# Kernel tuning notes

Measured on AMD Instinct MI355X. Metric: run time of the kernel, lower is better.

## Reference

```python
import jax, jax.numpy as jnp
import numpy as np


def _sage(x_src, x_dst, si, di, wl, b, wr):
    # out = x_dst @ wl^T + b  (self projection)
    out = x_dst @ wl.T + b
    n_dst = x_dst.shape[0]
    # mean aggregation of gathered source features over destination nodes
    agg = jax.ops.segment_sum(x_src[si], di, num_segments=n_dst)  # [N_dst, D]
    cnt = jax.ops.segment_sum(jnp.ones(si.shape, x_src.dtype), di, num_segments=n_dst)
    agg = agg / jnp.maximum(cnt, 1.0)[:, None]
    out = out + agg @ wr.T
    # F.normalize(p=2, dim=-1) with eps=1e-12
    norm = jnp.linalg.norm(out, axis=-1, keepdims=True)
    return out / jnp.maximum(norm, 1e-12)


def setup_inputs() -> dict:
    key = jax.random.key(0)
    ks = jax.random.split(key, 32)
    NA, NE, NF, D, E = 100000, 200000, 100000, 128, 400000
    inp = {
        'x_article': jax.random.normal(ks[0], (NA, D), jnp.float32),
        'x_entity': jax.random.normal(ks[1], (NE, D), jnp.float32),
        'x_fact': jax.random.normal(ks[2], (NF, D), jnp.float32),
    }
    # edge indices per EDGE_TYPES order
    srcs = [NA, NA, NE, NE, NF]
    dsts = [NE, NF, NA, NF, NE]
    for i in range(5):
        inp[f'si{i}'] = jax.random.randint(ks[3 + 2 * i], (E,), 0, srcs[i], jnp.int32)
        inp[f'di{i}'] = jax.random.randint(ks[4 + 2 * i], (E,), 0, dsts[i], jnp.int32)
    # per-edge-type params: W_l [out,in], b [out], W_r [out,in]
    scale = 1.0 / np.sqrt(D)
    for i in range(5):
        inp[f'wl{i}'] = jax.random.normal(ks[13 + 3 * i], (D, D), jnp.float32) * scale
        inp[f'b{i}'] = jnp.zeros((D,), jnp.float32)
        inp[f'wr{i}'] = jax.random.normal(ks[14 + 3 * i], (D, D), jnp.float32) * scale
    return inp


def reference(x_article, x_entity, x_fact,
              si0, di0, si1, di1, si2, di2, si3, di3, si4, di4,
              wl0, b0, wr0, wl1, b1, wr1, wl2, b2, wr2,
              wl3, b3, wr3, wl4, b4, wr4):
    # EDGE_TYPES: (article->entity), (article->fact), (entity->article),
    #             (entity->fact), (fact->entity); contributions to same dst are summed
    out_entity = _sage(x_article, x_entity, si0, di0, wl0, b0, wr0)
    out_fact = _sage(x_article, x_fact, si1, di1, wl1, b1, wr1)
    out_article = _sage(x_entity, x_article, si2, di2, wl2, b2, wr2)
    out_fact = out_fact + _sage(x_entity, x_fact, si3, di3, wl3, b3, wr3)
    out_entity = out_entity + _sage(x_fact, x_entity, si4, di4, wl4, b4, wr4)
    return out_article, out_entity, out_fact
```

## Files before the change

### kernel.cpp

```cpp
#include <hip/hip_runtime.h>
#include <hip/hip_bf16.h>

typedef __bf16 bf16;
typedef __attribute__((ext_vector_type(8))) __bf16 bf16x8;
typedef __attribute__((ext_vector_type(4))) float f32x4;

static __device__ inline bf16x8 pack_bf16x8(f32x4 lo, f32x4 hi) {
    bf16x8 t;
#pragma unroll
    for (int j = 0; j < 4; ++j) {
        t[j]     = (__bf16)lo[j];
        t[4 + j] = (__bf16)hi[j];
    }
    return t;
}

struct WConvArgs { const float* w[10]; bf16* dst; };

__global__ __launch_bounds__(256)
void convert_w(WConvArgs A) {
    int mat = blockIdx.y;
    int tid = blockIdx.x * 256 + threadIdx.x;
    if (tid >= 2048) return;
    int m  = tid & 15;
    int q  = (tid >> 4) & 3;
    int kc = (tid >> 6) & 3;
    int ct = tid >> 8;
    const float* src = A.w[mat] + (size_t)(ct * 16 + m) * 128 + kc * 32 + q * 8;
    bf16x8 t;
#pragma unroll
    for (int j = 0; j < 8; ++j) t[j] = (__bf16)src[j];
    bf16* dst = A.dst + (size_t)mat * 16384 + ((ct * 4 + kc) * 4 + q) * 128 + m * 8;
    *(bf16x8*)dst = t;
}

struct XConvArgs { const float* src[3]; bf16* dst[3]; long long n8[3]; };

__global__ __launch_bounds__(256)
void convert_x(XConvArgs A) {
    int a = blockIdx.y;
    const float* s = A.src[a];
    bf16* d = A.dst[a];
    long long n8 = A.n8[a];
    for (long long i = blockIdx.x * 256LL + threadIdx.x; i < n8;
         i += (long long)gridDim.x * 256) {
        const f32x4* p = (const f32x4*)(s + i * 8);
        ((bf16x8*)d)[i] = pack_bf16x8(p[0], p[1]);
    }
}

struct CsrArgs {
    const int* si[5];
    const int* di[5];
    int* ofs[5];
    int* tick[5];
    int* esrc[5];
    int* bsum[5];
    int E[5];
    int n1[5];
};

__global__ __launch_bounds__(256)
void csr_zero(CsrArgs A) {
    int t = blockIdx.y;
    int i = blockIdx.x * 256 + threadIdx.x;
    if (i < A.n1[t]) A.ofs[t][i] = 0;
}

__global__ __launch_bounds__(256)
void csr_hist(CsrArgs A) {
    int t = blockIdx.y;
    int E = A.E[t];
    const int* di = A.di[t];
    int* ofs = A.ofs[t];
    for (int i = blockIdx.x * 256 + threadIdx.x; i < E; i += gridDim.x * 256)
        atomicAdd(&ofs[di[i] + 1], 1);
}

__global__ __launch_bounds__(256)
void csr_scan_blocks(CsrArgs A) {
    __shared__ int lds[256];
    int ty = blockIdx.y;
    int n = A.n1[ty];
    int* a = A.ofs[ty];
    int* bsum = A.bsum[ty];
    int t = threadIdx.x;
    int base = blockIdx.x * 2048 + t * 8;
    int v[8];
    int run = 0;
#pragma unroll
    for (int j = 0; j < 8; ++j) {
        int idx = base + j;
        int x = (idx < n) ? a[idx] : 0;
        run += x;
        v[j] = run;
    }
    lds[t] = run;
    __syncthreads();
#pragma unroll
    for (int off = 1; off < 256; off <<= 1) {
        int x = (t >= off) ? lds[t - off] : 0;
        __syncthreads();
        lds[t] += x;
        __syncthreads();
    }
    int excl = t ? lds[t - 1] : 0;
#pragma unroll
    for (int j = 0; j < 8; ++j) {
        int idx = base + j;
        if (idx < n) a[idx] = v[j] + excl;
    }
    if (t == 255) bsum[blockIdx.x] = lds[255];
}

__global__ __launch_bounds__(256)
void csr_scan_bsums(CsrArgs A, int nb) {
    __shared__ int lds[256];
    int ty = blockIdx.x;
    int* bsum = A.bsum[ty];
    int t = threadIdx.x;
    int carry = 0;
    for (int base = 0; base < nb; base += 256) {
        int i = base + t;
        int v = (i < nb) ? bsum[i] : 0;
        lds[t] = v;
        __syncthreads();
#pragma unroll
        for (int off = 1; off < 256; off <<= 1) {
            int x = (t >= off) ? lds[t - off] : 0;
            __syncthreads();
            lds[t] += x;
            __syncthreads();
        }
        int excl = t ? lds[t - 1] : 0;
        if (i < nb) bsum[i] = excl + carry;
        carry += lds[255];
        __syncthreads();
    }
}

__global__ __launch_bounds__(256)
void csr_scan_add(CsrArgs A) {
    int ty = blockIdx.y;
    int n = A.n1[ty];
    int* a = A.ofs[ty];
    const int* bsum = A.bsum[ty];
    int* tick = A.tick[ty];
    int i = blockIdx.x * 256 + threadIdx.x;
    if (i < n) {
        int v = a[i] + bsum[i >> 11];
        a[i] = v;
        if (i < n - 1) tick[i] = v;
    }
}

__global__ __launch_bounds__(256)
void csr_fill(CsrArgs A) {
    int ty = blockIdx.y;
    int E = A.E[ty];
    const int* si = A.si[ty];
    const int* di = A.di[ty];
    int* tick = A.tick[ty];
    int* esrc = A.esrc[ty];
    for (int i = blockIdx.x * 256 + threadIdx.x; i < E; i += gridDim.x * 256) {
        int pos = atomicAdd(&tick[di[i]], 1);
        pos = pos < 0 ? 0 : (pos >= E ? E - 1 : pos);
        esrc[pos] = si[i];
    }
}

struct SageAll {
    int bend[3];
    int nd[3];
    int nc[3];
    const float* xdst_f[3];
    const bf16*  xdst_b[3];
    float* out[3];
    const float* xsrc_f[3][2];
    const bf16*  xsrc_b[3][2];
    const int* ofs[3][2];
    const int* esrc[3][2];
    const bf16* wf[3][2];
    const float* bias[3][2];
    int nsrc[3][2];
    int E[3][2];
};

template<int BF16S>
__global__ __launch_bounds__(256)
void sage_all(SageAll A) {
    int bid = blockIdx.x;
    int g = (bid >= A.bend[0]) + (bid >= A.bend[1]);
    int bloc = bid - (g ? A.bend[g - 1] : 0);
    int lane = threadIdx.x & 63;
    int wave = threadIdx.x >> 6;
    int m = lane & 15;
    int q = lane >> 4;
    int nd = A.nd[g];
    int r0 = bloc * 64 + wave * 16;
    int rl = min(r0 + m, nd - 1);

    bf16x8 a1[4];
    if constexpr (BF16S) {
        const bf16x8* xr = (const bf16x8*)(A.xdst_b[g] + (size_t)rl * 128);
#pragma unroll
        for (int kc = 0; kc < 4; ++kc) a1[kc] = xr[kc * 4 + q];
    } else {
        const f32x4* xrow = (const f32x4*)(A.xdst_f[g] + (size_t)rl * 128);
#pragma unroll
        for (int kc = 0; kc < 4; ++kc)
            a1[kc] = pack_bf16x8(xrow[kc * 8 + q * 2], xrow[kc * 8 + q * 2 + 1]);
    }

    float ysum[8][4];
#pragma unroll
    for (int ct = 0; ct < 8; ++ct)
#pragma unroll
        for (int r = 0; r < 4; ++r) ysum[ct][r] = 0.f;

    int nc = A.nc[g];
    for (int c = 0; c < nc; ++c) {
        const int* ofs  = A.ofs[g][c];
        const int* esrc = A.esrc[g][c];
        int nsrc = A.nsrc[g][c];
        int Et   = A.E[g][c];

        int start = ofs[rl];
        int end   = ofs[rl + 1];
        start = start < 0 ? 0 : (start > Et ? Et : start);
        end   = end < start ? start : (end > Et ? Et : end);

        f32x4 aglo[4], aghi[4];
#pragma unroll
        for (int kc = 0; kc < 4; ++kc) {
            aglo[kc] = (f32x4){0.f, 0.f, 0.f, 0.f};
            aghi[kc] = (f32x4){0.f, 0.f, 0.f, 0.f};
        }

        int e = start;
        if constexpr (BF16S) {
            const bf16* xs = A.xsrc_b[g][c];
            for (; e + 2 <= end; e += 2) {
                int s0 = esrc[e], s1 = esrc[e + 1];
                s0 = s0 < 0 ? 0 : (s0 >= nsrc ? nsrc - 1 : s0);
                s1 = s1 < 0 ? 0 : (s1 >= nsrc ? nsrc - 1 : s1);
                const bf16x8* p0 = (const bf16x8*)(xs + (size_t)s0 * 128);
                const bf16x8* p1 = (const bf16x8*)(xs + (size_t)s1 * 128);
#pragma unroll
                for (int kc = 0; kc < 4; ++kc) {
                    bf16x8 v0 = p0[kc * 4 + q];
                    bf16x8 v1 = p1[kc * 4 + q];
#pragma unroll
                    for (int j = 0; j < 4; ++j) {
                        aglo[kc][j] += (float)v0[j] + (float)v1[j];
                        aghi[kc][j] += (float)v0[4 + j] + (float)v1[4 + j];
                    }
                }
            }
            if (e < end) {
                int s0 = esrc[e];
                s0 = s0 < 0 ? 0 : (s0 >= nsrc ? nsrc - 1 : s0);
                const bf16x8* p0 = (const bf16x8*)(xs + (size_t)s0 * 128);
#pragma unroll
                for (int kc = 0; kc < 4; ++kc) {
                    bf16x8 v0 = p0[kc * 4 + q];
#pragma unroll
                    for (int j = 0; j < 4; ++j) {
                        aglo[kc][j] += (float)v0[j];
                        aghi[kc][j] += (float)v0[4 + j];
                    }
                }
            }
        } else {
            const float* xs = A.xsrc_f[g][c];
            for (; e + 2 <= end; e += 2) {
                int s0 = esrc[e], s1 = esrc[e + 1];
                s0 = s0 < 0 ? 0 : (s0 >= nsrc ? nsrc - 1 : s0);
                s1 = s1 < 0 ? 0 : (s1 >= nsrc ? nsrc - 1 : s1);
                const f32x4* p0 = (const f32x4*)(xs + (size_t)s0 * 128 + q * 8);
                const f32x4* p1 = (const f32x4*)(xs + (size_t)s1 * 128 + q * 8);
#pragma unroll
                for (int kc = 0; kc < 4; ++kc) {
                    aglo[kc] += p0[kc * 8] + p1[kc * 8];
                    aghi[kc] += p0[kc * 8 + 1] + p1[kc * 8 + 1];
                }
            }
            if (e < end) {
                int s0 = esrc[e];
                s0 = s0 < 0 ? 0 : (s0 >= nsrc ? nsrc - 1 : s0);
                const f32x4* p0 = (const f32x4*)(xs + (size_t)s0 * 128 + q * 8);
#pragma unroll
                for (int kc = 0; kc < 4; ++kc) {
                    aglo[kc] += p0[kc * 8];
                    aghi[kc] += p0[kc * 8 + 1];
                }
            }
        }

        float invc = 1.0f / (float)max(end - start, 1);
        bf16x8 a2[4];
#pragma unroll
        for (int kc = 0; kc < 4; ++kc) {
            bf16x8 t;
#pragma unroll
            for (int j = 0; j < 4; ++j) {
                t[j]     = (__bf16)(aglo[kc][j] * invc);
                t[4 + j] = (__bf16)(aghi[kc][j] * invc);
            }
            a2[kc] = t;
        }

        const bf16x8* wf = (const bf16x8*)A.wf[g][c];
        int fb = q * 16 + m;
        f32x4 acc[8];
#pragma unroll
        for (int ct = 0; ct < 8; ++ct) {
            f32x4 cc = {0.f, 0.f, 0.f, 0.f};
#pragma unroll
            for (int kc = 0; kc < 4; ++kc) {
                bf16x8 bl = wf[(ct * 4 + kc) * 64 + fb];
                bf16x8 br = wf[2048 + (ct * 4 + kc) * 64 + fb];
                cc = __builtin_amdgcn_mfma_f32_16x16x32_bf16(a1[kc], bl, cc, 0, 0, 0);
                cc = __builtin_amdgcn_mfma_f32_16x16x32_bf16(a2[kc], br, cc, 0, 0, 0);
            }
            acc[ct] = cc;
        }

        const float* bias = A.bias[g][c];
        float ss[4] = {0.f, 0.f, 0.f, 0.f};
#pragma unroll
        for (int ct = 0; ct < 8; ++ct) {
            float bb = bias[ct * 16 + m];
#pragma unroll
            for (int r = 0; r < 4; ++r) {
                float v = acc[ct][r] + bb;
                acc[ct][r] = v;
                ss[r] += v * v;
            }
        }
#pragma unroll
        for (int off = 1; off < 16; off <<= 1) {
#pragma unroll
            for (int r = 0; r < 4; ++r) ss[r] += __shfl_xor(ss[r], off);
        }
        float sc[4];
#pragma unroll
        for (int r = 0; r < 4; ++r) sc[r] = 1.0f / fmaxf(sqrtf(ss[r]), 1e-12f);
#pragma unroll
        for (int ct = 0; ct < 8; ++ct)
#pragma unroll
            for (int r = 0; r < 4; ++r) ysum[ct][r] += acc[ct][r] * sc[r];
    }

#pragma unroll
    for (int r = 0; r < 4; ++r) {
        int orow = r0 + q * 4 + r;
        if (orow < nd) {
            float* op = A.out[g] + (size_t)orow * 128 + m;
#pragma unroll
            for (int ct = 0; ct < 8; ++ct) op[ct * 16] = ysum[ct][r];
        }
    }
}

extern "C" void kernel_launch(void* const* d_in, const int* in_sizes, int n_in,
                              void* d_out, int out_size, void* d_ws, size_t ws_size,
                              hipStream_t stream) {
    const int D = 128;
    const float* xarr[3] = {(const float*)d_in[0], (const float*)d_in[1],
                            (const float*)d_in[2]};
    int NA = in_sizes[0] / D;
    int NE = in_sizes[1] / D;
    int NF = in_sizes[2] / D;
    int nrow[3] = {NA, NE, NF};

    const int* si[5];
    const int* di[5];
    int Et[5];
    for (int i = 0; i < 5; ++i) {
        si[i] = (const int*)d_in[3 + 2 * i];
        di[i] = (const int*)d_in[4 + 2 * i];
        Et[i] = in_sizes[3 + 2 * i];
    }
    const float *wl[5], *bia[5], *wr[5];
    for (int i = 0; i < 5; ++i) {
        wl[i]  = (const float*)d_in[13 + 3 * i];
        bia[i] = (const float*)d_in[14 + 3 * i];
        wr[i]  = (const float*)d_in[15 + 3 * i];
    }

    float* outp = (float*)d_out;
    float* grp_out[3] = {outp, outp + (size_t)NA * D, outp + (size_t)(NA + NE) * D};

    int xsrc_idx[5] = {0, 0, 1, 1, 2};
    int ndst[5]     = {NE, NF, NA, NF, NE};
    int grp_types[3][2] = {{2, -1}, {0, 4}, {1, 3}};
    int grp_nt[3]  = {1, 2, 2};
    int grp_nd[3]  = {NA, NE, NF};
    int grp_dst[3] = {0, 1, 2};

    size_t wf_bytes = (size_t)5 * 32768 * sizeof(bf16);
    size_t csr_all_ints = 0;
    for (int t = 0; t < 5; ++t)
        csr_all_ints += (size_t)(ndst[t] + 1) + ndst[t] + Et[t] + 128;
    size_t xb_elems = ((size_t)NA + NE + NF) * D;

    size_t off_csr = (wf_bytes + 15) & ~(size_t)15;
    size_t off_xb  = (off_csr + csr_all_ints * 4 + 15) & ~(size_t)15;
    int mode_full = (off_xb + xb_elems * sizeof(bf16)) <= ws_size;
    int mode_lean = (off_csr + csr_all_ints * 4) <= ws_size;

    bf16* wfrag = (bf16*)d_ws;
    WConvArgs wa;
    for (int t = 0; t < 5; ++t) {
        wa.w[t * 2]     = wl[t];
        wa.w[t * 2 + 1] = wr[t];
    }
    wa.dst = wfrag;
    convert_w<<<dim3(8, 10), 256, 0, stream>>>(wa);

    bf16* xb = (bf16*)((char*)d_ws + off_xb);
    bf16* xb_arr[3] = {xb, xb + (size_t)NA * D, xb + ((size_t)NA + NE) * D};
    if (mode_full) {
        XConvArgs xa;
        for (int a = 0; a < 3; ++a) {
            xa.src[a] = xarr[a];
            xa.dst[a] = xb_arr[a];
            xa.n8[a]  = (long long)nrow[a] * 16;
        }
        convert_x<<<dim3(2048, 3), 256, 0, stream>>>(xa);
    }

    int* type_ofs[5];
    int* type_esrc[5];
    auto run_csr = [&](const int* types, int nt, int* base) {
        CsrArgs ca = {};
        int* p = base;
        int max_n1 = 0;
        for (int k = 0; k < nt; ++k) {
            int t = types[k];
            int nd = ndst[t], n1 = nd + 1, E = Et[t];
            ca.si[k] = si[t];
            ca.di[k] = di[t];
            ca.ofs[k]  = p; p += n1;
            ca.tick[k] = p; p += nd;
            ca.esrc[k] = p; p += E;
            ca.bsum[k] = p; p += 128;
            ca.E[k] = E;
            ca.n1[k] = n1;
            if (n1 > max_n1) max_n1 = n1;
            type_ofs[t]  = ca.ofs[k];
            type_esrc[t] = ca.esrc[k];
        }
        int blk = (max_n1 + 255) / 256;
        int nb  = (max_n1 + 2047) / 2048;
        csr_zero<<<dim3(blk, nt), 256, 0, stream>>>(ca);
        csr_hist<<<dim3(1024, nt), 256, 0, stream>>>(ca);
        csr_scan_blocks<<<dim3(nb, nt), 256, 0, stream>>>(ca);
        csr_scan_bsums<<<dim3(nt), 256, 0, stream>>>(ca, nb);
        csr_scan_add<<<dim3(blk, nt), 256, 0, stream>>>(ca);
        csr_fill<<<dim3(1024, nt), 256, 0, stream>>>(ca);
    };

    auto fill_group = [&](SageAll& sa, int slot, int g) {
        sa.nd[slot] = grp_nd[g];
        sa.nc[slot] = grp_nt[g];
        sa.xdst_f[slot] = xarr[grp_dst[g]];
        sa.xdst_b[slot] = xb_arr[grp_dst[g]];
        sa.out[slot] = grp_out[g];
        for (int c = 0; c < grp_nt[g]; ++c) {
            int t = grp_types[g][c];
            sa.xsrc_f[slot][c] = xarr[xsrc_idx[t]];
            sa.xsrc_b[slot][c] = xb_arr[xsrc_idx[t]];
            sa.ofs[slot][c]  = type_ofs[t];
            sa.esrc[slot][c] = type_esrc[t];
            sa.wf[slot][c]   = wfrag + (size_t)t * 32768;
            sa.bias[slot][c] = bia[t];
            sa.nsrc[slot][c] = nrow[xsrc_idx[t]];
            sa.E[slot][c]    = Et[t];
        }
    };

    int* csr_base = (int*)((char*)d_ws + off_csr);

    if (mode_lean) {
        int all_types[5] = {0, 1, 2, 3, 4};
        run_csr(all_types, 5, csr_base);

        SageAll sa = {};
        int cum = 0;
        for (int g = 0; g < 3; ++g) {
            fill_group(sa, g, g);
            cum += (grp_nd[g] + 63) / 64;
            sa.bend[g] = cum;
        }
        if (mode_full)
            sage_all<1><<<cum, 256, 0, stream>>>(sa);
        else
            sage_all<0><<<cum, 256, 0, stream>>>(sa);
    } else {
        for (int g = 0; g < 3; ++g) {
            run_csr(grp_types[g], grp_nt[g], csr_base);
            SageAll sa = {};
            fill_group(sa, 0, g);
            int nb = (grp_nd[g] + 63) / 64;
            sa.bend[0] = nb; sa.bend[1] = nb; sa.bend[2] = nb;
            sage_all<0><<<nb, 256, 0, stream>>>(sa);
        }
    }
}
```

Before: 982.1 us.

## Replace CSR build with fixed-capacity per-destination buckets plus overflow list

```diff
diff --git a/kernel.cpp b/kernel.cpp
--- a/kernel.cpp
+++ b/kernel.cpp
@@ -46,6 +46,243 @@
          i += (long long)gridDim.x * 256) {
         const f32x4* p = (const f32x4*)(s + i * 8);
         ((bf16x8*)d)[i] = pack_bf16x8(p[0], p[1]);
+    }
+}
+
+struct FillArgs {
+    const int* si[5];
+    const int* di[5];
+    int* tick[5];
+    int* bucket[5];
+    int2* ovf[5];
+    int* ovfn[5];
+    int E[5];
+    int nd[5];
+    int C;
+};
+
+__global__ __launch_bounds__(256)
+void bkt_zero(FillArgs A) {
+    int t = blockIdx.y;
+    int nd = A.nd[t];
+    int* tick = A.tick[t];
+    for (int i = blockIdx.x * 256 + threadIdx.x; i < nd; i += gridDim.x * 256)
+        tick[i] = 0;
+    if (blockIdx.x == 0 && threadIdx.x == 0) *A.ovfn[t] = 0;
+}
+
+__global__ __launch_bounds__(256)
+void bkt_fill(FillArgs A) {
+    int t = blockIdx.y;
+    int E = A.E[t];
+    int nd = A.nd[t];
+    int C = A.C;
+    const int* si = A.si[t];
+    const int* di = A.di[t];
+    int* tick = A.tick[t];
+    int* bucket = A.bucket[t];
+    int2* ovf = A.ovf[t];
+    int* ovfn = A.ovfn[t];
+    for (int i = blockIdx.x * 256 + threadIdx.x; i < E; i += gridDim.x * 256) {
+        int d = di[i];
+        int s = si[i];
+        d = d < 0 ? 0 : (d >= nd ? nd - 1 : d);
+        int pos = atomicAdd(&tick[d], 1);
+        if (pos >= 0 && pos < C) {
+            bucket[(size_t)d * C + pos] = s;
+        } else {
+            int o = atomicAdd(ovfn, 1);
+            if (o >= 0 && o < E) ovf[o] = make_int2(d, s);
+        }
+    }
+}
+
+template<int BF16S>
+static __device__ inline void accum_src(const float* xf, const bf16* xb,
+                                        int s, int q, f32x4* aglo, f32x4* aghi) {
+    if constexpr (BF16S) {
+        const bf16x8* p = (const bf16x8*)(xb + (size_t)s * 128);
+#pragma unroll
+        for (int kc = 0; kc < 4; ++kc) {
+            bf16x8 v = p[kc * 4 + q];
+#pragma unroll
+            for (int j = 0; j < 4; ++j) {
+                aglo[kc][j] += (float)v[j];
+                aghi[kc][j] += (float)v[4 + j];
+            }
+        }
+    } else {
+        const f32x4* p = (const f32x4*)(xf + (size_t)s * 128 + q * 8);
+#pragma unroll
+        for (int kc = 0; kc < 4; ++kc) {
+            aglo[kc] += p[kc * 8];
+            aghi[kc] += p[kc * 8 + 1];
+        }
+    }
+}
+
+struct SageB {
+    int bend[3];
+    int nd[3];
+    int nc[3];
+    const float* xdst_f[3];
+    const bf16*  xdst_b[3];
+    float* out[3];
+    const float* xsrc_f[3][2];
+    const bf16*  xsrc_b[3][2];
+    const int* tick[3][2];
+    const int* bucket[3][2];
+    const int2* ovf[3][2];
+    const int* ovfn[3][2];
+    const bf16* wf[3][2];
+    const float* bias[3][2];
+    int nsrc[3][2];
+    int ovfcap[3][2];
+};
+
+template<int C, int BF16S>
+__global__ __launch_bounds__(256)
+void sage_bkt(SageB A) {
+    int bid = blockIdx.x;
+    int g = (bid >= A.bend[0]) + (bid >= A.bend[1]);
+    int bloc = bid - (g ? A.bend[g - 1] : 0);
+    int lane = threadIdx.x & 63;
+    int wave = threadIdx.x >> 6;
+    int m = lane & 15;
+    int q = lane >> 4;
+    int nd = A.nd[g];
+    int r0 = bloc * 64 + wave * 16;
+    int rl = min(r0 + m, nd - 1);
+
+    bf16x8 a1[4];
+    if constexpr (BF16S) {
+        const bf16x8* xr = (const bf16x8*)(A.xdst_b[g] + (size_t)rl * 128);
+#pragma unroll
+        for (int kc = 0; kc < 4; ++kc) a1[kc] = xr[kc * 4 + q];
+    } else {
+        const f32x4* xrow = (const f32x4*)(A.xdst_f[g] + (size_t)rl * 128);
+#pragma unroll
+        for (int kc = 0; kc < 4; ++kc)
+            a1[kc] = pack_bf16x8(xrow[kc * 8 + q * 2], xrow[kc * 8 + q * 2 + 1]);
+    }
+
+    float ysum[8][4];
+#pragma unroll
+    for (int ct = 0; ct < 8; ++ct)
+#pragma unroll
+        for (int r = 0; r < 4; ++r) ysum[ct][r] = 0.f;
+
+    int nc = A.nc[g];
+    for (int c = 0; c < nc; ++c) {
+        const float* xf = A.xsrc_f[g][c];
+        const bf16*  xb = A.xsrc_b[g][c];
+        int nsrc = A.nsrc[g][c];
+
+        int deg = A.tick[g][c][rl];
+        deg = deg < 0 ? 0 : deg;
+        int dc = deg < C ? deg : C;
+        const int* brow = A.bucket[g][c] + (size_t)rl * C;
+
+        f32x4 aglo[4], aghi[4];
+#pragma unroll
+        for (int kc = 0; kc < 4; ++kc) {
+            aglo[kc] = (f32x4){0.f, 0.f, 0.f, 0.f};
+            aghi[kc] = (f32x4){0.f, 0.f, 0.f, 0.f};
+        }
+
+#pragma unroll
+        for (int t0 = 0; t0 < C; t0 += 4) {
+            if (t0 < dc) {
+                int4 s4 = *(const int4*)(brow + t0);
+                int ss[4] = {s4.x, s4.y, s4.z, s4.w};
+#pragma unroll
+                for (int u = 0; u < 4; ++u) {
+                    if (t0 + u < dc) {
+                        int s = ss[u];
+                        s = s < 0 ? 0 : (s >= nsrc ? nsrc - 1 : s);
+                        accum_src<BF16S>(xf, xb, s, q, aglo, aghi);
+                    }
+                }
+            }
+        }
+        if (deg > C) {
+            int on = *A.ovfn[g][c];
+            int cap = A.ovfcap[g][c];
+            on = on < 0 ? 0 : (on > cap ? cap : on);
+            const int2* ov = A.ovf[g][c];
+            for (int i = 0; i < on; ++i) {
+                int2 ds = ov[i];
+                if (ds.x == rl) {
+                    int s = ds.y;
+                    s = s < 0 ? 0 : (s >= nsrc ? nsrc - 1 : s);
+                    accum_src<BF16S>(xf, xb, s, q, aglo, aghi);
+                }
+            }
+        }
+
+        float invc = 1.0f / (float)(deg > 0 ? deg : 1);
+        bf16x8 a2[4];
+#pragma unroll
+        for (int kc = 0; kc < 4; ++kc) {
+            bf16x8 t;
+#pragma unroll
+            for (int j = 0; j < 4; ++j) {
+                t[j]     = (__bf16)(aglo[kc][j] * invc);
+                t[4 + j] = (__bf16)(aghi[kc][j] * invc);
+            }
+            a2[kc] = t;
+        }
+
+        const bf16x8* wf = (const bf16x8*)A.wf[g][c];
+        int fb = q * 16 + m;
+        f32x4 acc[8];
+#pragma unroll
+        for (int ct = 0; ct < 8; ++ct) {
+            f32x4 cc = {0.f, 0.f, 0.f, 0.f};
+#pragma unroll
+            for (int kc = 0; kc < 4; ++kc) {
+                bf16x8 bl = wf[(ct * 4 + kc) * 64 + fb];
+                bf16x8 br = wf[2048 + (ct * 4 + kc) * 64 + fb];
+                cc = __builtin_amdgcn_mfma_f32_16x16x32_bf16(a1[kc], bl, cc, 0, 0, 0);
+                cc = __builtin_amdgcn_mfma_f32_16x16x32_bf16(a2[kc], br, cc, 0, 0, 0);
+            }
+            acc[ct] = cc;
+        }
+
+        const float* bias = A.bias[g][c];
+        float ss2[4] = {0.f, 0.f, 0.f, 0.f};
+#pragma unroll
+        for (int ct = 0; ct < 8; ++ct) {
+            float bb = bias[ct * 16 + m];
+#pragma unroll
+            for (int r = 0; r < 4; ++r) {
+                float v = acc[ct][r] + bb;
+                acc[ct][r] = v;
+                ss2[r] += v * v;
+            }
+        }
+#pragma unroll
+        for (int off = 1; off < 16; off <<= 1) {
+#pragma unroll
+            for (int r = 0; r < 4; ++r) ss2[r] += __shfl_xor(ss2[r], off);
+        }
+        float sc[4];
+#pragma unroll
+        for (int r = 0; r < 4; ++r) sc[r] = 1.0f / fmaxf(sqrtf(ss2[r]), 1e-12f);
+#pragma unroll
+        for (int ct = 0; ct < 8; ++ct)
+#pragma unroll
+            for (int r = 0; r < 4; ++r) ysum[ct][r] += acc[ct][r] * sc[r];
+    }
+
+#pragma unroll
+    for (int r = 0; r < 4; ++r) {
+        int orow = r0 + q * 4 + r;
+        if (orow < nd) {
+            float* op = A.out[g] + (size_t)orow * 128 + m;
+#pragma unroll
+            for (int ct = 0; ct < 8; ++ct) op[ct * 16] = ysum[ct][r];
+        }
     }
 }
 
@@ -174,10 +411,8 @@
     int nd[3];
     int nc[3];
     const float* xdst_f[3];
-    const bf16*  xdst_b[3];
     float* out[3];
     const float* xsrc_f[3][2];
-    const bf16*  xsrc_b[3][2];
     const int* ofs[3][2];
     const int* esrc[3][2];
     const bf16* wf[3][2];
@@ -186,7 +421,6 @@
     int E[3][2];
 };
 
-template<int BF16S>
 __global__ __launch_bounds__(256)
 void sage_all(SageAll A) {
     int bid = blockIdx.x;
@@ -201,16 +435,10 @@
     int rl = min(r0 + m, nd - 1);
 
     bf16x8 a1[4];
-    if constexpr (BF16S) {
-        const bf16x8* xr = (const bf16x8*)(A.xdst_b[g] + (size_t)rl * 128);
-#pragma unroll
-        for (int kc = 0; kc < 4; ++kc) a1[kc] = xr[kc * 4 + q];
-    } else {
-        const f32x4* xrow = (const f32x4*)(A.xdst_f[g] + (size_t)rl * 128);
-#pragma unroll
-        for (int kc = 0; kc < 4; ++kc)
-            a1[kc] = pack_bf16x8(xrow[kc * 8 + q * 2], xrow[kc * 8 + q * 2 + 1]);
-    }
+    const f32x4* xrow = (const f32x4*)(A.xdst_f[g] + (size_t)rl * 128);
+#pragma unroll
+    for (int kc = 0; kc < 4; ++kc)
+        a1[kc] = pack_bf16x8(xrow[kc * 8 + q * 2], xrow[kc * 8 + q * 2 + 1]);
 
     float ysum[8][4];
 #pragma unroll
@@ -236,65 +464,10 @@
             aglo[kc] = (f32x4){0.f, 0.f, 0.f, 0.f};
             aghi[kc] = (f32x4){0.f, 0.f, 0.f, 0.f};
         }
-
-        int e = start;
-        if constexpr (BF16S) {
-            const bf16* xs = A.xsrc_b[g][c];
-            for (; e + 2 <= end; e += 2) {
-                int s0 = esrc[e], s1 = esrc[e + 1];
-                s0 = s0 < 0 ? 0 : (s0 >= nsrc ? nsrc - 1 : s0);
-                s1 = s1 < 0 ? 0 : (s1 >= nsrc ? nsrc - 1 : s1);
-                const bf16x8* p0 = (const bf16x8*)(xs + (size_t)s0 * 128);
-                const bf16x8* p1 = (const bf16x8*)(xs + (size_t)s1 * 128);
-#pragma unroll
-                for (int kc = 0; kc < 4; ++kc) {
-                    bf16x8 v0 = p0[kc * 4 + q];
-                    bf16x8 v1 = p1[kc * 4 + q];
-#pragma unroll
-                    for (int j = 0; j < 4; ++j) {
-                        aglo[kc][j] += (float)v0[j] + (float)v1[j];
-                        aghi[kc][j] += (float)v0[4 + j] + (float)v1[4 + j];
-                    }
-                }
-            }
-            if (e < end) {
-                int s0 = esrc[e];
-                s0 = s0 < 0 ? 0 : (s0 >= nsrc ? nsrc - 1 : s0);
-                const bf16x8* p0 = (const bf16x8*)(xs + (size_t)s0 * 128);
-#pragma unroll
-                for (int kc = 0; kc < 4; ++kc) {
-                    bf16x8 v0 = p0[kc * 4 + q];
-#pragma unroll
-                    for (int j = 0; j < 4; ++j) {
-                        aglo[kc][j] += (float)v0[j];
-                        aghi[kc][j] += (float)v0[4 + j];
-                    }
-                }
-            }
-        } else {
-            const float* xs = A.xsrc_f[g][c];
-            for (; e + 2 <= end; e += 2) {
-                int s0 = esrc[e], s1 = esrc[e + 1];
-                s0 = s0 < 0 ? 0 : (s0 >= nsrc ? nsrc - 1 : s0);
-                s1 = s1 < 0 ? 0 : (s1 >= nsrc ? nsrc - 1 : s1);
-                const f32x4* p0 = (const f32x4*)(xs + (size_t)s0 * 128 + q * 8);
-                const f32x4* p1 = (const f32x4*)(xs + (size_t)s1 * 128 + q * 8);
-#pragma unroll
-                for (int kc = 0; kc < 4; ++kc) {
-                    aglo[kc] += p0[kc * 8] + p1[kc * 8];
-                    aghi[kc] += p0[kc * 8 + 1] + p1[kc * 8 + 1];
-                }
-            }
-            if (e < end) {
-                int s0 = esrc[e];
-                s0 = s0 < 0 ? 0 : (s0 >= nsrc ? nsrc - 1 : s0);
-                const f32x4* p0 = (const f32x4*)(xs + (size_t)s0 * 128 + q * 8);
-#pragma unroll
-                for (int kc = 0; kc < 4; ++kc) {
-                    aglo[kc] += p0[kc * 8];
-                    aghi[kc] += p0[kc * 8 + 1];
-                }
-            }
+        for (int e = start; e < end; ++e) {
+            int s = esrc[e];
+            s = s < 0 ? 0 : (s >= nsrc ? nsrc - 1 : s);
+            accum_src<0>(A.xsrc_f[g][c], nullptr, s, q, aglo, aghi);
         }
 
         float invc = 1.0f / (float)max(end - start, 1);
@@ -327,7 +500,7 @@
         }
 
         const float* bias = A.bias[g][c];
-        float ss[4] = {0.f, 0.f, 0.f, 0.f};
+        float ss2[4] = {0.f, 0.f, 0.f, 0.f};
 #pragma unroll
         for (int ct = 0; ct < 8; ++ct) {
             float bb = bias[ct * 16 + m];
@@ -335,17 +508,17 @@
             for (int r = 0; r < 4; ++r) {
                 float v = acc[ct][r] + bb;
                 acc[ct][r] = v;
-                ss[r] += v * v;
+                ss2[r] += v * v;
             }
         }
 #pragma unroll
         for (int off = 1; off < 16; off <<= 1) {
 #pragma unroll
-            for (int r = 0; r < 4; ++r) ss[r] += __shfl_xor(ss[r], off);
+            for (int r = 0; r < 4; ++r) ss2[r] += __shfl_xor(ss2[r], off);
         }
         float sc[4];
 #pragma unroll
-        for (int r = 0; r < 4; ++r) sc[r] = 1.0f / fmaxf(sqrtf(ss[r]), 1e-12f);
+        for (int r = 0; r < 4; ++r) sc[r] = 1.0f / fmaxf(sqrtf(ss2[r]), 1e-12f);
 #pragma unroll
         for (int ct = 0; ct < 8; ++ct)
 #pragma unroll
@@ -400,15 +573,7 @@
     int grp_dst[3] = {0, 1, 2};
 
     size_t wf_bytes = (size_t)5 * 32768 * sizeof(bf16);
-    size_t csr_all_ints = 0;
-    for (int t = 0; t < 5; ++t)
-        csr_all_ints += (size_t)(ndst[t] + 1) + ndst[t] + Et[t] + 128;
     size_t xb_elems = ((size_t)NA + NE + NF) * D;
-
-    size_t off_csr = (wf_bytes + 15) & ~(size_t)15;
-    size_t off_xb  = (off_csr + csr_all_ints * 4 + 15) & ~(size_t)15;
-    int mode_full = (off_xb + xb_elems * sizeof(bf16)) <= ws_size;
-    int mode_lean = (off_csr + csr_all_ints * 4) <= ws_size;
 
     bf16* wfrag = (bf16*)d_ws;
     WConvArgs wa;
@@ -419,17 +584,98 @@
     wa.dst = wfrag;
     convert_w<<<dim3(8, 10), 256, 0, stream>>>(wa);
 
-    bf16* xb = (bf16*)((char*)d_ws + off_xb);
-    bf16* xb_arr[3] = {xb, xb + (size_t)NA * D, xb + ((size_t)NA + NE) * D};
-    if (mode_full) {
-        XConvArgs xa;
-        for (int a = 0; a < 3; ++a) {
-            xa.src[a] = xarr[a];
-            xa.dst[a] = xb_arr[a];
-            xa.n8[a]  = (long long)nrow[a] * 16;
-        }
-        convert_x<<<dim3(2048, 3), 256, 0, stream>>>(xa);
-    }
+    struct BktLayout {
+        size_t tick[5], ovfn[5], bkt[5], ovf[5], xb, end;
+    };
+    auto layout_bkt = [&](int C, int want_xb, BktLayout& L) -> bool {
+        size_t p = (wf_bytes + 63) & ~(size_t)63;
+        for (int t = 0; t < 5; ++t) {
+            L.tick[t] = p; p += (size_t)ndst[t] * 4;
+            L.ovfn[t] = p; p += 64;
+            L.bkt[t] = p; p += (size_t)ndst[t] * C * 4;
+            p = (p + 15) & ~(size_t)15;
+            L.ovf[t] = p; p += (size_t)Et[t] * 8;
+            p = (p + 15) & ~(size_t)15;
+        }
+        L.xb = p;
+        if (want_xb) p += xb_elems * sizeof(bf16);
+        L.end = p;
+        return p <= ws_size;
+    };
+
+    BktLayout L;
+    int C = 0, use_xb = 0;
+    if (layout_bkt(16, 1, L))      { C = 16; use_xb = 1; }
+    else if (layout_bkt(8, 1, L))  { C = 8;  use_xb = 1; }
+    else if (layout_bkt(16, 0, L)) { C = 16; use_xb = 0; }
+    else if (layout_bkt(8, 0, L))  { C = 8;  use_xb = 0; }
+
+    if (C > 0) {
+        bf16* xb = (bf16*)((char*)d_ws + L.xb);
+        bf16* xb_arr[3] = {xb, xb + (size_t)NA * D, xb + ((size_t)NA + NE) * D};
+        if (use_xb) {
+            XConvArgs xa;
+            for (int a = 0; a < 3; ++a) {
+                xa.src[a] = xarr[a];
+                xa.dst[a] = xb_arr[a];
+                xa.n8[a]  = (long long)nrow[a] * 16;
+            }
+            convert_x<<<dim3(2048, 3), 256, 0, stream>>>(xa);
+        }
+
+        FillArgs fa = {};
+        int max_nd = 0;
+        for (int t = 0; t < 5; ++t) {
+            fa.si[t] = si[t];
+            fa.di[t] = di[t];
+            fa.tick[t]   = (int*)((char*)d_ws + L.tick[t]);
+            fa.bucket[t] = (int*)((char*)d_ws + L.bkt[t]);
+            fa.ovf[t]    = (int2*)((char*)d_ws + L.ovf[t]);
+            fa.ovfn[t]   = (int*)((char*)d_ws + L.ovfn[t]);
+            fa.E[t] = Et[t];
+            fa.nd[t] = ndst[t];
+            if (ndst[t] > max_nd) max_nd = ndst[t];
+        }
+        fa.C = C;
+        bkt_zero<<<dim3((max_nd + 255) / 256, 5), 256, 0, stream>>>(fa);
+        bkt_fill<<<dim3(1024, 5), 256, 0, stream>>>(fa);
+
+        SageB sb = {};
+        int cum = 0;
+        for (int g = 0; g < 3; ++g) {
+            sb.nd[g] = grp_nd[g];
+            sb.nc[g] = grp_nt[g];
+            sb.xdst_f[g] = xarr[grp_dst[g]];
+            sb.xdst_b[g] = xb_arr[grp_dst[g]];
+            sb.out[g] = grp_out[g];
+            for (int c = 0; c < grp_nt[g]; ++c) {
+                int t = grp_types[g][c];
+                sb.xsrc_f[g][c] = xarr[xsrc_idx[t]];
+                sb.xsrc_b[g][c] = xb_arr[xsrc_idx[t]];
+                sb.tick[g][c]   = fa.tick[t];
+                sb.bucket[g][c] = fa.bucket[t];
+                sb.ovf[g][c]    = fa.ovf[t];
+                sb.ovfn[g][c]   = fa.ovfn[t];
+                sb.wf[g][c]     = wfrag + (size_t)t * 32768;
+                sb.bias[g][c]   = bia[t];
+                sb.nsrc[g][c]   = nrow[xsrc_idx[t]];
+                sb.ovfcap[g][c] = Et[t];
+            }
+            cum += (grp_nd[g] + 63) / 64;
+            sb.bend[g] = cum;
+        }
+        if (C == 16 && use_xb)       sage_bkt<16, 1><<<cum, 256, 0, stream>>>(sb);
+        else if (C == 8 && use_xb)   sage_bkt<8, 1><<<cum, 256, 0, stream>>>(sb);
+        else if (C == 16)            sage_bkt<16, 0><<<cum, 256, 0, stream>>>(sb);
+        else                         sage_bkt<8, 0><<<cum, 256, 0, stream>>>(sb);
+        return;
+    }
+
+    size_t csr_all_ints = 0;
+    for (int t = 0; t < 5; ++t)
+        csr_all_ints += (size_t)(ndst[t] + 1) + ndst[t] + Et[t] + 128;
+    size_t off_csr = (wf_bytes + 15) & ~(size_t)15;
+    int mode_lean = (off_csr + csr_all_ints * 4) <= ws_size;
 
     int* type_ofs[5];
     int* type_esrc[5];
@@ -466,12 +712,10 @@
         sa.nd[slot] = grp_nd[g];
         sa.nc[slot] = grp_nt[g];
         sa.xdst_f[slot] = xarr[grp_dst[g]];
-        sa.xdst_b[slot] = xb_arr[grp_dst[g]];
         sa.out[slot] = grp_out[g];
         for (int c = 0; c < grp_nt[g]; ++c) {
             int t = grp_types[g][c];
             sa.xsrc_f[slot][c] = xarr[xsrc_idx[t]];
-            sa.xsrc_b[slot][c] = xb_arr[xsrc_idx[t]];
             sa.ofs[slot][c]  = type_ofs[t];
             sa.esrc[slot][c] = type_esrc[t];
             sa.wf[slot][c]   = wfrag + (size_t)t * 32768;
@@ -482,11 +726,9 @@
     };
 
     int* csr_base = (int*)((char*)d_ws + off_csr);
-
     if (mode_lean) {
         int all_types[5] = {0, 1, 2, 3, 4};
         run_csr(all_types, 5, csr_base);
-
         SageAll sa = {};
         int cum = 0;
         for (int g = 0; g < 3; ++g) {
@@ -494,10 +736,7 @@
             cum += (grp_nd[g] + 63) / 64;
             sa.bend[g] = cum;
         }
-        if (mode_full)
-            sage_all<1><<<cum, 256, 0, stream>>>(sa);
-        else
-            sage_all<0><<<cum, 256, 0, stream>>>(sa);
+        sage_all<<<cum, 256, 0, stream>>>(sa);
     } else {
         for (int g = 0; g < 3; ++g) {
             run_csr(grp_types[g], grp_nt[g], csr_base);
@@ -505,7 +744,7 @@
             fill_group(sa, 0, g);
             int nb = (grp_nd[g] + 63) / 64;
             sa.bend[0] = nb; sa.bend[1] = nb; sa.bend[2] = nb;
-            sage_all<0><<<nb, 256, 0, stream>>>(sa);
-        }
-    }
-}
+            sage_all<<<nb, 256, 0, stream>>>(sa);
+        }
+    }
+}
```

Result: faster. 857.7 us (-12.7%).
